# Kernel optimization log

Measured on AMD Instinct MI355X. Metric: run time of the kernel, lower is better.

Reference implementation:

```python
import jax, jax.numpy as jnp
import numpy as np

B, S, D = 4, 2048, 2048
H = 16
DH = D // H  # 128

def _rope_tables(seq_len, d_head, base=10000.0):
    inv_freq = 1.0 / (base ** (np.arange(0, d_head, 2, dtype=np.float32) / d_head))
    pos = np.arange(seq_len, dtype=np.float32)
    ang = pos[:, None] * inv_freq[None, :]  # (S, d_head/2)
    return jnp.asarray(np.cos(ang)), jnp.asarray(np.sin(ang))

def setup_inputs() -> dict:
    key = jax.random.key(0)
    ks = jax.random.split(key, 4)
    x = jax.random.normal(ks[0], (B, S, D), dtype=jnp.float32)
    rope_cos, rope_sin = _rope_tables(S, DH)
    # Linear params, scaled like torch default init (~1/sqrt(fan_in))
    Wqkv = jax.random.normal(ks[1], (D, 3 * D), dtype=jnp.float32) / np.sqrt(D)
    bqkv = jnp.zeros((3 * D,), dtype=jnp.float32)
    Wout = jax.random.normal(ks[2], (D, D), dtype=jnp.float32) / np.sqrt(D)
    bout = jnp.zeros((D,), dtype=jnp.float32)
    return {"x": x, "rope_cos": rope_cos, "rope_sin": rope_sin,
            "Wqkv": Wqkv, "bqkv": bqkv, "Wout": Wout, "bout": bout}

def _apply_rope(x, cos, sin):
    # x: (B, H, S, DH); cos/sin: (S, DH/2), broadcast over B,H
    x1 = x[..., 0::2]
    x2 = x[..., 1::2]
    out = jnp.stack([x1 * cos - x2 * sin, x1 * sin + x2 * cos], axis=-1)
    return out.reshape(*out.shape[:-2], -1)  # interleave back to (..., DH)

def reference(x, rope_cos, rope_sin, Wqkv, bqkv, Wout, bout):
    qkv = (x @ Wqkv + bqkv).reshape(B, S, 3, H, DH)
    qkv = jnp.transpose(qkv, (2, 0, 3, 1, 4))  # (3, B, H, S, DH)
    q, k, v = qkv[0], qkv[1], qkv[2]
    q = _apply_rope(q, rope_cos, rope_sin)
    k = _apply_rope(k, rope_cos, rope_sin)
    scale = 1.0 / np.sqrt(DH)
    scores = jnp.einsum('bhqd,bhkd->bhqk', q, k) * scale  # (B,H,S,S)
    causal = jnp.tril(jnp.ones((S, S), dtype=bool))
    scores = jnp.where(causal, scores, jnp.finfo(scores.dtype).min)
    attn = jax.nn.softmax(scores, axis=-1)
    out = jnp.einsum('bhqk,bhkd->bhqd', attn, v)  # (B,H,S,DH)
    out = jnp.transpose(out, (0, 2, 1, 3)).reshape(B, S, D)
    return out @ Wout + bout
```

## Files before the change

kernel.cpp:

```cpp
#include <hip/hip_runtime.h>
#include <hip/hip_bf16.h>
#include <math.h>

typedef __attribute__((ext_vector_type(8))) short bf16x8;
typedef __attribute__((ext_vector_type(4))) float f32x4;
typedef __attribute__((ext_vector_type(16))) float f32x16;
typedef __attribute__((ext_vector_type(8))) unsigned short u16x8;
typedef __attribute__((ext_vector_type(4))) unsigned short u16x4;

static constexpr int B = 4, S = 2048, D = 2048, H = 16, DH = 128;
static constexpr int N3 = 3 * D;
static constexpr int M = B * S;

__device__ __forceinline__ unsigned short f2bf(float f) {
  unsigned u = __float_as_uint(f);
  u += 0x7fffu + ((u >> 16) & 1u);
  return (unsigned short)(u >> 16);
}
__device__ __forceinline__ float bf2f(unsigned short b) {
  return __uint_as_float(((unsigned)b) << 16);
}

__global__ __launch_bounds__(256) void cvt_kernel(const float* __restrict__ in,
                                                  unsigned short* __restrict__ out) {
  size_t i = (size_t)blockIdx.x * 256 + threadIdx.x;
  f32x4 v = *(const f32x4*)(in + i * 4);
  u16x4 o;
  o[0] = f2bf(v[0]); o[1] = f2bf(v[1]); o[2] = f2bf(v[2]); o[3] = f2bf(v[3]);
  *(u16x4*)(out + i * 4) = o;
}

__global__ __launch_bounds__(256) void transpose_kernel(const float* __restrict__ W,
                                                        unsigned short* __restrict__ WT,
                                                        int K, int N) {
  __shared__ float t[32][33];
  int tx = threadIdx.x, ty = threadIdx.y;
  int n0 = blockIdx.x * 32, k0 = blockIdx.y * 32;
#pragma unroll
  for (int i = 0; i < 4; i++)
    t[ty + i * 8][tx] = W[(size_t)(k0 + ty + i * 8) * N + n0 + tx];
  __syncthreads();
#pragma unroll
  for (int i = 0; i < 4; i++)
    WT[(size_t)(n0 + ty + i * 8) * K + k0 + tx] = f2bf(t[tx][ty + i * 8]);
}

__device__ __forceinline__ void gload_lds(const void* g, void* l) {
  __builtin_amdgcn_global_load_lds((const __attribute__((address_space(1))) void*)g,
                                   (__attribute__((address_space(3))) void*)l, 16, 0, 0);
}

template <int EPI>
__global__ __launch_bounds__(512, 1) void gemm_bt(
    const unsigned short* __restrict__ A, const unsigned short* __restrict__ Bt,
    const float* __restrict__ bias, float* __restrict__ Cf,
    unsigned short* __restrict__ Qp, unsigned short* __restrict__ Kp,
    unsigned short* __restrict__ VTp, int Nn, int nbn) {
  __shared__ __align__(16) unsigned short lds[65536];
  constexpr int NT = 32;
  const int tid = threadIdx.x;
  const int l = tid & 63;
  const int w = tid >> 6;
  const int lc = l & 15, lr = l >> 4;
  const int wm = w >> 2, wn = w & 3;

  const int nwg = gridDim.x;
  const int cpx = nwg >> 3;
  const int wg = blockIdx.x;
  const int swz = (wg & 7) * cpx + (wg >> 3);
  const int bm = swz / nbn;
  const int bn = swz - bm * nbn;

  const int lq = l >> 2, lg = l & 3;
  const int gsw = lg ^ ((l >> 3) & 3);
  const unsigned short* sA[2];
  const unsigned short* sB[2];
  int dA[2], dB[2];
#pragma unroll
  for (int mh = 0; mh < 2; mh++) {
    const int rowA = mh * 64 + wn * 16 + lq;
    sA[mh] = A + (size_t)(bm * 256 + wm * 128 + rowA) * 2048 + gsw * 8;
    dA[mh] = wm * 8192 + rowA * 32 + lg * 8;
    const int rowB = (wm * 2 + (wn & 1)) * 32 + mh * 16 + lq;
    sB[mh] = Bt + (size_t)(bn * 256 + (wn >> 1) * 128 + rowB) * 2048 + gsw * 8;
    dB[mh] = 32768 + (wn >> 1) * 8192 + rowB * 32 + lg * 8;
  }

  const int rsw = (lr ^ ((lc >> 1) & 3)) * 8;
  const int frA = wm * 8192 + lc * 32 + rsw;
  const int frB = 32768 + (wn >> 1) * 8192 + ((wn & 1) * 64 + lc) * 32 + rsw;

  f32x4 acc[8][4];
#pragma unroll
  for (int m = 0; m < 8; m++)
#pragma unroll
    for (int n = 0; n < 4; n++) acc[m][n] = (f32x4)0.f;

#define STG(t1, kh, mh)                                                          \
  do {                                                                           \
    const int dbo_ = ((t1) & 1) * 16384 + (kh) * 4096;                           \
    const int ko_ = (t1) * 64 + (kh) * 32;                                       \
    gload_lds(sA[mh] + ko_, lds + dbo_ + dA[mh]);                                \
    gload_lds(sB[mh] + ko_, lds + dbo_ + dB[mh]);                                \
  } while (0)

  STG(0, 0, 0); STG(0, 0, 1); STG(0, 1, 0); STG(0, 1, 1);
  __builtin_amdgcn_sched_barrier(0);
  asm volatile("s_waitcnt vmcnt(0)" ::: "memory");
  __builtin_amdgcn_s_barrier();
  __builtin_amdgcn_sched_barrier(0);

  bf16x8 bfr[4];

#define PHASE(db, kh, mh, DOSTG, t1)                                             \
  do {                                                                           \
    bf16x8 af0, af1, af2, af3;                                                   \
    const int ab_ = (db) * 16384 + (kh) * 4096 + frA + (mh) * 2048;              \
    af0 = *(const bf16x8*)(lds + ab_);                                           \
    af1 = *(const bf16x8*)(lds + ab_ + 512);                                     \
    af2 = *(const bf16x8*)(lds + ab_ + 1024);                                    \
    af3 = *(const bf16x8*)(lds + ab_ + 1536);                                    \
    if (mh == 0) {                                                               \
      const int bb_ = (db) * 16384 + (kh) * 4096 + frB;                          \
      bfr[0] = *(const bf16x8*)(lds + bb_);                                      \
      bfr[1] = *(const bf16x8*)(lds + bb_ + 512);                                \
      bfr[2] = *(const bf16x8*)(lds + bb_ + 1024);                               \
      bfr[3] = *(const bf16x8*)(lds + bb_ + 1536);                               \
    }                                                                            \
    if (DOSTG) STG(t1, kh, mh);                                                  \
    __builtin_amdgcn_sched_barrier(0);                                           \
    asm volatile("s_waitcnt lgkmcnt(0)" ::: "memory");                           \
    __builtin_amdgcn_sched_barrier(0);                                           \
    __builtin_amdgcn_s_setprio(1);                                               \
    _Pragma("unroll")                                                            \
    for (int nt = 0; nt < 4; nt++) {                                             \
      acc[(mh)*4 + 0][nt] = __builtin_amdgcn_mfma_f32_16x16x32_bf16(af0, bfr[nt], acc[(mh)*4 + 0][nt], 0, 0, 0); \
      acc[(mh)*4 + 1][nt] = __builtin_amdgcn_mfma_f32_16x16x32_bf16(af1, bfr[nt], acc[(mh)*4 + 1][nt], 0, 0, 0); \
      acc[(mh)*4 + 2][nt] = __builtin_amdgcn_mfma_f32_16x16x32_bf16(af2, bfr[nt], acc[(mh)*4 + 2][nt], 0, 0, 0); \
      acc[(mh)*4 + 3][nt] = __builtin_amdgcn_mfma_f32_16x16x32_bf16(af3, bfr[nt], acc[(mh)*4 + 3][nt], 0, 0, 0); \
    }                                                                            \
    __builtin_amdgcn_s_setprio(0);                                               \
    __builtin_amdgcn_sched_barrier(0);                                           \
    asm volatile("s_waitcnt vmcnt(4)" ::: "memory");                             \
    __builtin_amdgcn_s_barrier();                                                \
    __builtin_amdgcn_sched_barrier(0);                                           \
  } while (0)

#pragma unroll 2
  for (int t = 0; t < NT; t++) {
    const int db = t & 1;
    const bool dg = (t + 1) < NT;
    PHASE(db, 0, 0, dg, t + 1);
    PHASE(db, 0, 1, dg, t + 1);
    PHASE(db, 1, 0, dg, t + 1);
    PHASE(db, 1, 1, dg, t + 1);
  }
#undef PHASE
#undef STG

#pragma unroll
  for (int m = 0; m < 8; m++) {
#pragma unroll
    for (int n = 0; n < 4; n++) {
      const int col = bn * 256 + wn * 64 + n * 16 + lc;
      const float bv = bias[col];
#pragma unroll
      for (int r = 0; r < 4; r++) {
        const int row = bm * 256 + wm * 128 + (m >> 2) * 64 + (m & 3) * 16 + lr * 4 + r;
        const float v = acc[m][n][r] + bv;
        if (EPI == 0) {
          const unsigned short ob = f2bf(v);
          const int b = row >> 11, s = row & 2047;
          const int which = col >> 11, within = col & 2047;
          const int h = within >> 7, d = within & 127;
          const size_t bh = (size_t)(b * H + h);
          if (which == 0)      Qp[(bh * S + s) * DH + d] = ob;
          else if (which == 1) Kp[(bh * S + s) * DH + d] = ob;
          else                 VTp[(bh * DH + d) * S + s] = ob;
        } else {
          Cf[(size_t)row * Nn + col] = v;
        }
      }
    }
  }
}

__global__ __launch_bounds__(256) void rope_kernel(unsigned short* __restrict__ T,
                                                   const float* __restrict__ cosT,
                                                   const float* __restrict__ sinT) {
  int t = blockIdx.x * 256 + threadIdx.x;
  int d8 = t & 15;
  int s = (t >> 4) & (S - 1);
  size_t off = (size_t)t * 8;
  u16x8 v = *(const u16x8*)(T + off);
  f32x4 c = *(const f32x4*)(cosT + (size_t)s * (DH / 2) + d8 * 4);
  f32x4 sn = *(const f32x4*)(sinT + (size_t)s * (DH / 2) + d8 * 4);
  u16x8 o;
#pragma unroll
  for (int j = 0; j < 4; j++) {
    float x1 = bf2f(v[2 * j]), x2 = bf2f(v[2 * j + 1]);
    o[2 * j]     = f2bf(x1 * c[j] - x2 * sn[j]);
    o[2 * j + 1] = f2bf(x1 * sn[j] + x2 * c[j]);
  }
  *(u16x8*)(T + off) = o;
}

__global__ __launch_bounds__(512, 1) void attn4_kernel(
    const unsigned short* __restrict__ Q, const unsigned short* __restrict__ Kt,
    const unsigned short* __restrict__ VT, unsigned short* __restrict__ O) {
  __shared__ __align__(16) unsigned short lK[2][64 * 128];
  __shared__ __align__(16) unsigned short lV[2][128 * 72];
  const int tid = threadIdx.x;
  const int w = tid >> 6;
  const int l = tid & 63;
  const int ql = l & 31;
  const int hi = l >> 5;
  const int j = blockIdx.x;
  const int bh = ((j >> 3) & 7) * 8 + (j & 7);
  const int pr = j >> 6;
  const int b = bh >> 4, h = bh & 15;
  const size_t base = (size_t)bh * S * DH;
  const float cl = 0.088388347648318447f * 1.44269504088896341f;

  const unsigned short* Ksrc[2];
  int Kdst[2];
#pragma unroll
  for (int i = 0; i < 2; i++) {
    const int g = i * 512 + tid;
    const int krow = g >> 4;
    Ksrc[i] = Kt + base + (size_t)krow * 128 + (g & 15) * 8;
    Kdst[i] = (g * 8) ^ ((krow & 7) << 3);
  }
  const int vdh = tid >> 2;
  const unsigned short* Vsrc = VT + ((size_t)bh * DH + vdh) * S;
  int vcol[2], Vdst[2];
#pragma unroll
  for (int i = 0; i < 2; i++) {
    vcol[i] = (tid & 3) * 8 + i * 32;
    Vdst[i] = vdh * 72 + vcol[i];
  }
  const int sfx = (ql & 7) << 3;

  for (int half = 0; half < 2; half++) {
    const int strip = half ? 7 - pr : pr;
    const int qw0 = strip * 256 + w * 32;

    bf16x8 qf[8];
    const unsigned short* qp = Q + base + (size_t)(qw0 + ql) * DH + hi * 8;
#pragma unroll
    for (int t = 0; t < 8; t++) qf[t] = *(const bf16x8*)(qp + t * 16);

    f32x16 acc[4];
#pragma unroll
    for (int mt = 0; mt < 4; mt++) acc[mt] = (f32x16)0.f;
    float m = -INFINITY, lsum = 0.f;

    const int ntb = 4 * (strip + 1);

    {
      f32x4 k0 = *(const f32x4*)(Ksrc[0]);
      f32x4 k1 = *(const f32x4*)(Ksrc[1]);
      f32x4 v0 = *(const f32x4*)(Vsrc + vcol[0]);
      f32x4 v1 = *(const f32x4*)(Vsrc + vcol[1]);
      *(f32x4*)(&lK[0][Kdst[0]]) = k0;
      *(f32x4*)(&lK[0][Kdst[1]]) = k1;
      *(f32x4*)(&lV[0][Vdst[0]]) = v0;
      *(f32x4*)(&lV[0][Vdst[1]]) = v1;
      __syncthreads();
    }

    for (int kb = 0; kb < ntb; kb++) {
      const int cur = kb & 1;
      const bool more = (kb + 1 < ntb);
      f32x4 k0r, k1r, v0r, v1r;
      if (more) {
        k0r = *(const f32x4*)(Ksrc[0] + (size_t)(kb + 1) * 8192);
        k1r = *(const f32x4*)(Ksrc[1] + (size_t)(kb + 1) * 8192);
        v0r = *(const f32x4*)(Vsrc + (kb + 1) * 64 + vcol[0]);
        v1r = *(const f32x4*)(Vsrc + (kb + 1) * 64 + vcol[1]);
      }
      const unsigned short* kbuf = lK[cur];
      const unsigned short* vbuf = lV[cur];
#pragma unroll
      for (int stx = 0; stx < 2; stx++) {
        const int kvs = kb * 64 + stx * 32;
        if (kvs <= qw0) {
          const bool diag = (kvs == qw0);
          const int krb = (stx * 32 + ql) * 128;
          f32x16 s0 = (f32x16)0.f, s1 = (f32x16)0.f;
#pragma unroll
          for (int t = 0; t < 4; t++) {
            bf16x8 k0 = *(const bf16x8*)(kbuf + ((krb + (2 * t) * 16 + 8 * hi) ^ sfx));
            bf16x8 k1 = *(const bf16x8*)(kbuf + ((krb + (2 * t + 1) * 16 + 8 * hi) ^ sfx));
            s0 = __builtin_amdgcn_mfma_f32_32x32x16_bf16(k0, qf[2 * t], s0, 0, 0, 0);
            s1 = __builtin_amdgcn_mfma_f32_32x32x16_bf16(k1, qf[2 * t + 1], s1, 0, 0, 0);
          }
          float sv[16];
#pragma unroll
          for (int r = 0; r < 16; r++) sv[r] = s0[r] + s1[r];
          if (diag) {
#pragma unroll
            for (int r = 0; r < 16; r++) {
              const int klocal = (r & 3) + 8 * (r >> 2) + 4 * hi;
              sv[r] = (klocal > ql) ? -INFINITY : sv[r];
            }
          }
          float smax = sv[0];
#pragma unroll
          for (int r = 1; r < 16; r++) smax = fmaxf(smax, sv[r]);
          smax = fmaxf(smax, __shfl_xor(smax, 32));

          float fr = 1.f;
          if (!__all((smax - m) * cl <= 8.0f)) {
            const float mn = fmaxf(m, smax);
            fr = exp2f((m - mn) * cl);
            m = mn;
#pragma unroll
            for (int mt = 0; mt < 4; mt++)
#pragma unroll
              for (int r = 0; r < 16; r++) acc[mt][r] *= fr;
          }
          float p[16];
          float ps = 0.f;
#pragma unroll
          for (int r = 0; r < 16; r++) {
            p[r] = exp2f((sv[r] - m) * cl);
            ps += p[r];
          }
          lsum = lsum * fr + ps + __shfl_xor(ps, 32);

          unsigned W[8];
#pragma unroll
          for (int qd = 0; qd < 4; qd++) {
            W[2 * qd]     = (unsigned)f2bf(p[4 * qd])     | ((unsigned)f2bf(p[4 * qd + 1]) << 16);
            W[2 * qd + 1] = (unsigned)f2bf(p[4 * qd + 2]) | ((unsigned)f2bf(p[4 * qd + 3]) << 16);
          }
#pragma unroll
          for (int t = 0; t < 2; t++) {
            const unsigned ss0 = hi ? W[4 * t] : W[4 * t + 2];
            const unsigned ss1 = hi ? W[4 * t + 1] : W[4 * t + 3];
            const unsigned r0 = __shfl_xor((int)ss0, 32);
            const unsigned r1 = __shfl_xor((int)ss1, 32);
            union { unsigned u[4]; bf16x8 v; } pf;
            if (hi == 0) { pf.u[0] = W[4 * t]; pf.u[1] = W[4 * t + 1]; pf.u[2] = r0; pf.u[3] = r1; }
            else         { pf.u[0] = r0; pf.u[1] = r1; pf.u[2] = W[4 * t + 2]; pf.u[3] = W[4 * t + 3]; }
#pragma unroll
            for (int mt = 0; mt < 4; mt++) {
              const bf16x8 vf = *(const bf16x8*)(vbuf + (mt * 32 + ql) * 72 + stx * 32 + 16 * t + 8 * hi);
              acc[mt] = __builtin_amdgcn_mfma_f32_32x32x16_bf16(vf, pf.v, acc[mt], 0, 0, 0);
            }
          }
        }
      }
      if (more) {
        *(f32x4*)(&lK[cur ^ 1][Kdst[0]]) = k0r;
        *(f32x4*)(&lK[cur ^ 1][Kdst[1]]) = k1r;
        *(f32x4*)(&lV[cur ^ 1][Vdst[0]]) = v0r;
        *(f32x4*)(&lV[cur ^ 1][Vdst[1]]) = v1r;
      }
      __syncthreads();
    }

    const float inv = 1.f / lsum;
    const int s_glob = qw0 + ql;
    unsigned short* op = O + ((size_t)(b * S + s_glob) * H + h) * DH;
#pragma unroll
    for (int mt = 0; mt < 4; mt++)
#pragma unroll
      for (int g = 0; g < 4; g++) {
        u16x4 ov;
#pragma unroll
        for (int jj = 0; jj < 4; jj++) ov[jj] = f2bf(acc[mt][4 * g + jj] * inv);
        *(u16x4*)(op + mt * 32 + 8 * g + 4 * hi) = ov;
      }
  }
}

extern "C" void kernel_launch(void* const* d_in, const int* in_sizes, int n_in,
                              void* d_out, int out_size, void* d_ws, size_t ws_size,
                              hipStream_t stream) {
  const float* x    = (const float*)d_in[0];
  const float* cosT = (const float*)d_in[1];
  const float* sinT = (const float*)d_in[2];
  const float* Wqkv = (const float*)d_in[3];
  const float* bqkv = (const float*)d_in[4];
  const float* Wout = (const float*)d_in[5];
  const float* bout = (const float*)d_in[6];

  char* ws = (char*)d_ws;
  unsigned short* xbf   = (unsigned short*)(ws);
  unsigned short* WqkvT = (unsigned short*)(ws + ((size_t)32 << 20));
  unsigned short* WoutT = (unsigned short*)(ws + ((size_t)56 << 20));
  unsigned short* VTb   = (unsigned short*)(ws + ((size_t)64 << 20));
  unsigned short* Qb = (unsigned short*)d_out;
  unsigned short* Kb = (unsigned short*)d_out + (size_t)M * D;
  unsigned short* Ob = xbf;

  cvt_kernel<<<M * D / 1024, 256, 0, stream>>>(x, xbf);
  transpose_kernel<<<dim3(N3 / 32, D / 32), dim3(32, 8), 0, stream>>>(Wqkv, WqkvT, D, N3);
  transpose_kernel<<<dim3(D / 32, D / 32), dim3(32, 8), 0, stream>>>(Wout, WoutT, D, D);
  gemm_bt<0><<<dim3((M / 256) * (N3 / 256)), 512, 0, stream>>>(xbf, WqkvT, bqkv, nullptr,
                                                               Qb, Kb, VTb, N3, N3 / 256);
  rope_kernel<<<(B * H * S * 16) / 256, 256, 0, stream>>>(Qb, cosT, sinT);
  rope_kernel<<<(B * H * S * 16) / 256, 256, 0, stream>>>(Kb, cosT, sinT);
  attn4_kernel<<<B * H * 4, 512, 0, stream>>>(Qb, Kb, VTb, Ob);
  gemm_bt<1><<<dim3((M / 256) * (D / 256)), 512, 0, stream>>>(Ob, WoutT, bout, (float*)d_out,
                                                              nullptr, nullptr, nullptr, D, D / 256);
}
```

Measured before the change: 489.4 us.

## Fuse RoPE into attention kernel loads and tree-reduce softmax max/sum

Removes the two standalone RoPE kernels and applies the rotation inside the attention kernel. Q is rotated as it is loaded into registers, and K is rotated while it is staged from global memory into LDS. This avoids a full read-modify-write pass over Q and K plus two kernel launches. In exchange, K is re-rotated by every block that loads it, which adds extra cos/sin global loads and more live registers in the prefetch path. The row max and sum reductions also become balanced trees to shorten dependency chains.

Result: no change. 495.6 us (+1.3%).

```diff
diff --git a/kernel.cpp b/kernel.cpp
--- a/kernel.cpp
+++ b/kernel.cpp
@@ -19,6 +19,18 @@
 }
 __device__ __forceinline__ float bf2f(unsigned short b) {
   return __uint_as_float(((unsigned)b) << 16);
+}
+
+__device__ __forceinline__ f32x4 rope8(f32x4 raw, f32x4 c, f32x4 sn) {
+  union { f32x4 f; unsigned short u[8]; } a, o;
+  a.f = raw;
+#pragma unroll
+  for (int j = 0; j < 4; j++) {
+    const float x1 = bf2f(a.u[2 * j]), x2 = bf2f(a.u[2 * j + 1]);
+    o.u[2 * j]     = f2bf(x1 * c[j] - x2 * sn[j]);
+    o.u[2 * j + 1] = f2bf(x1 * sn[j] + x2 * c[j]);
+  }
+  return o.f;
 }
 
 __global__ __launch_bounds__(256) void cvt_kernel(const float* __restrict__ in,
@@ -185,29 +197,10 @@
   }
 }
 
-__global__ __launch_bounds__(256) void rope_kernel(unsigned short* __restrict__ T,
-                                                   const float* __restrict__ cosT,
-                                                   const float* __restrict__ sinT) {
-  int t = blockIdx.x * 256 + threadIdx.x;
-  int d8 = t & 15;
-  int s = (t >> 4) & (S - 1);
-  size_t off = (size_t)t * 8;
-  u16x8 v = *(const u16x8*)(T + off);
-  f32x4 c = *(const f32x4*)(cosT + (size_t)s * (DH / 2) + d8 * 4);
-  f32x4 sn = *(const f32x4*)(sinT + (size_t)s * (DH / 2) + d8 * 4);
-  u16x8 o;
-#pragma unroll
-  for (int j = 0; j < 4; j++) {
-    float x1 = bf2f(v[2 * j]), x2 = bf2f(v[2 * j + 1]);
-    o[2 * j]     = f2bf(x1 * c[j] - x2 * sn[j]);
-    o[2 * j + 1] = f2bf(x1 * sn[j] + x2 * c[j]);
-  }
-  *(u16x8*)(T + off) = o;
-}
-
-__global__ __launch_bounds__(512, 1) void attn4_kernel(
+__global__ __launch_bounds__(512, 1) void attn5_kernel(
     const unsigned short* __restrict__ Q, const unsigned short* __restrict__ Kt,
-    const unsigned short* __restrict__ VT, unsigned short* __restrict__ O) {
+    const unsigned short* __restrict__ VT, unsigned short* __restrict__ O,
+    const float* __restrict__ cosT, const float* __restrict__ sinT) {
   __shared__ __align__(16) unsigned short lK[2][64 * 128];
   __shared__ __align__(16) unsigned short lV[2][128 * 72];
   const int tid = threadIdx.x;
@@ -223,12 +216,16 @@
   const float cl = 0.088388347648318447f * 1.44269504088896341f;
 
   const unsigned short* Ksrc[2];
+  const float* Kcos[2];
+  const float* Ksin[2];
   int Kdst[2];
 #pragma unroll
   for (int i = 0; i < 2; i++) {
     const int g = i * 512 + tid;
     const int krow = g >> 4;
     Ksrc[i] = Kt + base + (size_t)krow * 128 + (g & 15) * 8;
+    Kcos[i] = cosT + (size_t)krow * 64 + (g & 15) * 4;
+    Ksin[i] = sinT + (size_t)krow * 64 + (g & 15) * 4;
     Kdst[i] = (g * 8) ^ ((krow & 7) << 3);
   }
   const int vdh = tid >> 2;
@@ -246,9 +243,21 @@
     const int qw0 = strip * 256 + w * 32;
 
     bf16x8 qf[8];
-    const unsigned short* qp = Q + base + (size_t)(qw0 + ql) * DH + hi * 8;
-#pragma unroll
-    for (int t = 0; t < 8; t++) qf[t] = *(const bf16x8*)(qp + t * 16);
+    {
+      const int sq = qw0 + ql;
+      const unsigned short* qp = Q + base + (size_t)sq * DH + hi * 8;
+      const float* cq = cosT + (size_t)sq * 64 + hi * 4;
+      const float* sq_ = sinT + (size_t)sq * 64 + hi * 4;
+#pragma unroll
+      for (int t = 0; t < 8; t++) {
+        f32x4 raw = *(const f32x4*)(qp + t * 16);
+        f32x4 c = *(const f32x4*)(cq + t * 8);
+        f32x4 sn = *(const f32x4*)(sq_ + t * 8);
+        union { f32x4 f; bf16x8 v; } u;
+        u.f = rope8(raw, c, sn);
+        qf[t] = u.v;
+      }
+    }
 
     f32x16 acc[4];
 #pragma unroll
@@ -258,8 +267,10 @@
     const int ntb = 4 * (strip + 1);
 
     {
-      f32x4 k0 = *(const f32x4*)(Ksrc[0]);
-      f32x4 k1 = *(const f32x4*)(Ksrc[1]);
+      f32x4 k0 = rope8(*(const f32x4*)(Ksrc[0]), *(const f32x4*)(Kcos[0]),
+                       *(const f32x4*)(Ksin[0]));
+      f32x4 k1 = rope8(*(const f32x4*)(Ksrc[1]), *(const f32x4*)(Kcos[1]),
+                       *(const f32x4*)(Ksin[1]));
       f32x4 v0 = *(const f32x4*)(Vsrc + vcol[0]);
       f32x4 v1 = *(const f32x4*)(Vsrc + vcol[1]);
       *(f32x4*)(&lK[0][Kdst[0]]) = k0;
@@ -272,10 +283,14 @@
     for (int kb = 0; kb < ntb; kb++) {
       const int cur = kb & 1;
       const bool more = (kb + 1 < ntb);
-      f32x4 k0r, k1r, v0r, v1r;
+      f32x4 k0r, k1r, v0r, v1r, c0r, c1r, s0r, s1r;
       if (more) {
         k0r = *(const f32x4*)(Ksrc[0] + (size_t)(kb + 1) * 8192);
         k1r = *(const f32x4*)(Ksrc[1] + (size_t)(kb + 1) * 8192);
+        c0r = *(const f32x4*)(Kcos[0] + (size_t)(kb + 1) * 4096);
+        c1r = *(const f32x4*)(Kcos[1] + (size_t)(kb + 1) * 4096);
+        s0r = *(const f32x4*)(Ksin[0] + (size_t)(kb + 1) * 4096);
+        s1r = *(const f32x4*)(Ksin[1] + (size_t)(kb + 1) * 4096);
         v0r = *(const f32x4*)(Vsrc + (kb + 1) * 64 + vcol[0]);
         v1r = *(const f32x4*)(Vsrc + (kb + 1) * 64 + vcol[1]);
       }
@@ -305,9 +320,12 @@
               sv[r] = (klocal > ql) ? -INFINITY : sv[r];
             }
           }
-          float smax = sv[0];
-#pragma unroll
-          for (int r = 1; r < 16; r++) smax = fmaxf(smax, sv[r]);
+          float t8[8];
+#pragma unroll
+          for (int r = 0; r < 8; r++) t8[r] = fmaxf(sv[r], sv[r + 8]);
+          float t4a = fmaxf(t8[0], t8[4]), t4b = fmaxf(t8[1], t8[5]);
+          float t4c = fmaxf(t8[2], t8[6]), t4d = fmaxf(t8[3], t8[7]);
+          float smax = fmaxf(fmaxf(t4a, t4b), fmaxf(t4c, t4d));
           smax = fmaxf(smax, __shfl_xor(smax, 32));
 
           float fr = 1.f;
@@ -321,12 +339,14 @@
               for (int r = 0; r < 16; r++) acc[mt][r] *= fr;
           }
           float p[16];
-          float ps = 0.f;
-#pragma unroll
-          for (int r = 0; r < 16; r++) {
-            p[r] = exp2f((sv[r] - m) * cl);
-            ps += p[r];
-          }
+#pragma unroll
+          for (int r = 0; r < 16; r++) p[r] = exp2f((sv[r] - m) * cl);
+          float a8[8];
+#pragma unroll
+          for (int r = 0; r < 8; r++) a8[r] = p[r] + p[r + 8];
+          float a4a = a8[0] + a8[4], a4b = a8[1] + a8[5];
+          float a4c = a8[2] + a8[6], a4d = a8[3] + a8[7];
+          float ps = (a4a + a4b) + (a4c + a4d);
           lsum = lsum * fr + ps + __shfl_xor(ps, 32);
 
           unsigned W[8];
@@ -353,8 +373,8 @@
         }
       }
       if (more) {
-        *(f32x4*)(&lK[cur ^ 1][Kdst[0]]) = k0r;
-        *(f32x4*)(&lK[cur ^ 1][Kdst[1]]) = k1r;
+        *(f32x4*)(&lK[cur ^ 1][Kdst[0]]) = rope8(k0r, c0r, s0r);
+        *(f32x4*)(&lK[cur ^ 1][Kdst[1]]) = rope8(k1r, c1r, s1r);
         *(f32x4*)(&lV[cur ^ 1][Vdst[0]]) = v0r;
         *(f32x4*)(&lV[cur ^ 1][Vdst[1]]) = v1r;
       }
@@ -401,9 +421,7 @@
   transpose_kernel<<<dim3(D / 32, D / 32), dim3(32, 8), 0, stream>>>(Wout, WoutT, D, D);
   gemm_bt<0><<<dim3((M / 256) * (N3 / 256)), 512, 0, stream>>>(xbf, WqkvT, bqkv, nullptr,
                                                                Qb, Kb, VTb, N3, N3 / 256);
-  rope_kernel<<<(B * H * S * 16) / 256, 256, 0, stream>>>(Qb, cosT, sinT);
-  rope_kernel<<<(B * H * S * 16) / 256, 256, 0, stream>>>(Kb, cosT, sinT);
-  attn4_kernel<<<B * H * 4, 512, 0, stream>>>(Qb, Kb, VTb, Ob);
+  attn5_kernel<<<B * H * 4, 512, 0, stream>>>(Qb, Kb, VTb, Ob, cosT, sinT);
   gemm_bt<1><<<dim3((M / 256) * (D / 256)), 512, 0, stream>>>(Ob, WoutT, bout, (float*)d_out,
                                                               nullptr, nullptr, nullptr, D, D / 256);
 }
```
